# Performance work log

Hardware: AMD Instinct MI355X
Metric: run time of the kernel (lower is better)

## Reference

```python
import jax, jax.numpy as jnp
import numpy as np

B, H = 65536, 256  # batch, hidden_size (== input_size since combine = input + hidden)


def setup_inputs() -> dict:
    key = jax.random.key(0)
    ks = jax.random.split(key, 11)
    s = 1.0 / np.sqrt(H)  # nn.Linear default init scale
    return {
        "input": jax.random.normal(ks[0], (B, H), jnp.float32),
        "hidden": jax.random.normal(ks[1], (B, H), jnp.float32),
        "cell": jax.random.normal(ks[2], (B, H), jnp.float32),
        "Wf": jax.random.uniform(ks[3], (H, H), jnp.float32, -s, s),
        "bf": jax.random.uniform(ks[4], (H,), jnp.float32, -s, s),
        "Wc": jax.random.uniform(ks[5], (H, H), jnp.float32, -s, s),
        "bc": jax.random.uniform(ks[6], (H,), jnp.float32, -s, s),
        "Wi": jax.random.uniform(ks[7], (H, H), jnp.float32, -s, s),
        "bi": jax.random.uniform(ks[8], (H,), jnp.float32, -s, s),
        "Wo": jax.random.uniform(ks[9], (H, H), jnp.float32, -s, s),
        "bo": jax.random.uniform(ks[10], (H,), jnp.float32, -s, s),
    }


def reference(input, hidden, cell, Wf, bf, Wc, bc, Wi, bi, Wo, bo):
    combine = input + hidden                                   # [B, H]
    ft = jax.nn.sigmoid(combine @ Wf.T + bf)                   # forget gate
    ct_ = jnp.tanh(combine @ Wc.T + bc)                        # candidate
    it = jax.nn.sigmoid(jax.nn.sigmoid(combine @ Wi.T + bi))   # note: double sigmoid, as in source
    cell_state = cell * ft + ct_ * it                          # [B, H]
    out = jax.nn.sigmoid(combine @ Wo.T + bo)                  # output gate
    hidden_state = out * jnp.tanh(cell_state)
    return (out, hidden_state, cell_state)
```

## Files before the change

### kernel.cpp

```cpp
#include <hip/hip_runtime.h>
#include <hip/hip_bf16.h>


typedef __attribute__((ext_vector_type(8))) short short8;
typedef __attribute__((ext_vector_type(4))) float f32x4;

static constexpr int Bsz  = 65536;
static constexpr int Hdim = 256;

__device__ __forceinline__ short f2bf(float f) {
    unsigned u = __float_as_uint(f);
    return (short)((u + 0x7FFFu + ((u >> 16) & 1u)) >> 16);
}
__device__ __forceinline__ float fast_rcp(float x) {
    float r;
    asm("v_rcp_f32 %0, %1" : "=v"(r) : "v"(x));
    return r;
}
__device__ __forceinline__ float sigm(float x) {
    return fast_rcp(1.0f + __expf(-x));
}
__device__ __forceinline__ float tanh_fast(float x) {
    return 2.0f * fast_rcp(1.0f + __expf(-2.0f * x)) - 1.0f;
}

__global__ void __launch_bounds__(256)
prep_w_kernel(const float* __restrict__ Wf, const float* __restrict__ Wc,
              const float* __restrict__ Wi, const float* __restrict__ Wo,
              short* __restrict__ Bp)
{
    int o    = blockIdx.x * 256 + threadIdx.x;
    int e    = o & 7;
    int lane = (o >> 3) & 63;
    int jf   = (o >> 9) & 15;
    int ks   = (o >> 13) & 7;
    int g    = (o >> 16) & 3;
    int k = ks * 32 + (lane >> 4) * 8 + e;
    int j = jf * 16 + (lane & 15);
    const float* W = (g == 0) ? Wf : (g == 1) ? Wc : (g == 2) ? Wi : Wo;
    Bp[o] = f2bf(W[j * 256 + k]);
}

__global__ void __launch_bounds__(256, 4)
lstm_main(const float* __restrict__ inp, const float* __restrict__ hid,
          const float* __restrict__ cell, const short* __restrict__ Bp,
          const float* __restrict__ bfv, const float* __restrict__ bcv,
          const float* __restrict__ biv, const float* __restrict__ bov,
          float* __restrict__ out)
{
    __shared__ short As[32 * 256];

    const int tid  = threadIdx.x;
    const int lane = tid & 63;
    const int wave = tid >> 6;
    const int lm   = lane & 15;
    const int lk   = lane >> 4;

    const int bid     = blockIdx.x;
    const int jq      = (bid >> 3) & 3;
    const int rowtile = (bid >> 5) * 8 + (bid & 7);
    const int rowblk  = rowtile * 32;

    const int j         = jq * 64 + wave * 16 + lm;
    const int jf_global = jq * 4 + wave;

    float4 Li[4][2], Lh[4][2];
#pragma unroll
    for (int c = 0; c < 4; ++c) {
        int cc  = tid + c * 256;
        int row = cc >> 5;
        int k0  = (cc & 31) * 8;
        const float4* ip = reinterpret_cast<const float4*>(inp + (size_t)(rowblk + row) * Hdim + k0);
        const float4* hp = reinterpret_cast<const float4*>(hid + (size_t)(rowblk + row) * Hdim + k0);
        Li[c][0] = ip[0]; Li[c][1] = ip[1];
        Lh[c][0] = hp[0]; Lh[c][1] = hp[1];
    }
    float cv[2][4];
#pragma unroll
    for (int mf = 0; mf < 2; ++mf)
#pragma unroll
        for (int r = 0; r < 4; ++r)
            cv[mf][r] = cell[(size_t)(rowblk + mf * 16 + lk * 4 + r) * Hdim + j];
    const float bF = bfv[j], bC = bcv[j], bI = biv[j], bO = bov[j];

#pragma unroll
    for (int c = 0; c < 4; ++c) {
        int cc  = tid + c * 256;
        int row = cc >> 5;
        int k0  = (cc & 31) * 8;
        short8 v;
        v[0] = f2bf(Li[c][0].x + Lh[c][0].x);
        v[1] = f2bf(Li[c][0].y + Lh[c][0].y);
        v[2] = f2bf(Li[c][0].z + Lh[c][0].z);
        v[3] = f2bf(Li[c][0].w + Lh[c][0].w);
        v[4] = f2bf(Li[c][1].x + Lh[c][1].x);
        v[5] = f2bf(Li[c][1].y + Lh[c][1].y);
        v[6] = f2bf(Li[c][1].z + Lh[c][1].z);
        v[7] = f2bf(Li[c][1].w + Lh[c][1].w);
        int byte = (row * 512 + k0 * 2) ^ ((row & 7) << 4);
        *reinterpret_cast<short8*>(reinterpret_cast<char*>(As) + byte) = v;
    }

    __syncthreads();

    f32x4 acc[4][2];
    acc[0][0] = (f32x4){bF, bF, bF, bF};
    acc[1][0] = (f32x4){bC, bC, bC, bC};
    acc[2][0] = (f32x4){bI, bI, bI, bI};
    acc[3][0] = (f32x4){bO, bO, bO, bO};
#pragma unroll
    for (int g = 0; g < 4; ++g) acc[g][1] = acc[g][0];

    const char* A = reinterpret_cast<const char*>(As);
    auto wload = [&](int g, int ks) -> short8 {
        int chunk = (g * 8 + ks) * 16 + jf_global;
        return *reinterpret_cast<const short8*>(Bp + ((size_t)chunk * 64 + lane) * 8);
    };
    auto aload = [&](int mf, int ks) -> short8 {
        int row  = mf * 16 + lm;
        int byte = (row * 512 + (ks * 32 + lk * 8) * 2) ^ ((row & 7) << 4);
        return *reinterpret_cast<const short8*>(A + byte);
    };

    short8 bA0 = wload(0, 0), bA1 = wload(1, 0), bA2 = wload(2, 0), bA3 = wload(3, 0);

#pragma unroll
    for (int ks2 = 0; ks2 < 8; ks2 += 2) {
        short8 cf0[2] = { aload(0, ks2), aload(1, ks2) };
        short8 bB0 = wload(0, ks2 + 1), bB1 = wload(1, ks2 + 1),
               bB2 = wload(2, ks2 + 1), bB3 = wload(3, ks2 + 1);
        acc[0][0] = __builtin_amdgcn_mfma_f32_16x16x32_bf16(cf0[0], bA0, acc[0][0], 0, 0, 0);
        acc[0][1] = __builtin_amdgcn_mfma_f32_16x16x32_bf16(cf0[1], bA0, acc[0][1], 0, 0, 0);
        acc[1][0] = __builtin_amdgcn_mfma_f32_16x16x32_bf16(cf0[0], bA1, acc[1][0], 0, 0, 0);
        acc[1][1] = __builtin_amdgcn_mfma_f32_16x16x32_bf16(cf0[1], bA1, acc[1][1], 0, 0, 0);
        acc[2][0] = __builtin_amdgcn_mfma_f32_16x16x32_bf16(cf0[0], bA2, acc[2][0], 0, 0, 0);
        acc[2][1] = __builtin_amdgcn_mfma_f32_16x16x32_bf16(cf0[1], bA2, acc[2][1], 0, 0, 0);
        acc[3][0] = __builtin_amdgcn_mfma_f32_16x16x32_bf16(cf0[0], bA3, acc[3][0], 0, 0, 0);
        acc[3][1] = __builtin_amdgcn_mfma_f32_16x16x32_bf16(cf0[1], bA3, acc[3][1], 0, 0, 0);

        short8 cf1[2] = { aload(0, ks2 + 1), aload(1, ks2 + 1) };
        if (ks2 + 2 < 8) {
            bA0 = wload(0, ks2 + 2); bA1 = wload(1, ks2 + 2);
            bA2 = wload(2, ks2 + 2); bA3 = wload(3, ks2 + 2);
        }
        acc[0][0] = __builtin_amdgcn_mfma_f32_16x16x32_bf16(cf1[0], bB0, acc[0][0], 0, 0, 0);
        acc[0][1] = __builtin_amdgcn_mfma_f32_16x16x32_bf16(cf1[1], bB0, acc[0][1], 0, 0, 0);
        acc[1][0] = __builtin_amdgcn_mfma_f32_16x16x32_bf16(cf1[0], bB1, acc[1][0], 0, 0, 0);
        acc[1][1] = __builtin_amdgcn_mfma_f32_16x16x32_bf16(cf1[1], bB1, acc[1][1], 0, 0, 0);
        acc[2][0] = __builtin_amdgcn_mfma_f32_16x16x32_bf16(cf1[0], bB2, acc[2][0], 0, 0, 0);
        acc[2][1] = __builtin_amdgcn_mfma_f32_16x16x32_bf16(cf1[1], bB2, acc[2][1], 0, 0, 0);
        acc[3][0] = __builtin_amdgcn_mfma_f32_16x16x32_bf16(cf1[0], bB3, acc[3][0], 0, 0, 0);
        acc[3][1] = __builtin_amdgcn_mfma_f32_16x16x32_bf16(cf1[1], bB3, acc[3][1], 0, 0, 0);
    }

    float* out0 = out;
    float* out1 = out + (size_t)Bsz * Hdim;
    float* out2 = out + (size_t)2 * Bsz * Hdim;

#pragma unroll
    for (int mf = 0; mf < 2; ++mf) {
#pragma unroll
        for (int r = 0; r < 4; ++r) {
            int row = rowblk + mf * 16 + lk * 4 + r;
            size_t off = (size_t)row * Hdim + j;
            float F = sigm(acc[0][mf][r]);
            float C = tanh_fast(acc[1][mf][r]);
            float I = sigm(sigm(acc[2][mf][r]));
            float O = sigm(acc[3][mf][r]);
            float cs = cv[mf][r] * F + C * I;
            float hs = O * tanh_fast(cs);
            out0[off] = O;
            out1[off] = hs;
            out2[off] = cs;
        }
    }
}

extern "C" void kernel_launch(void* const* d_in, const int* in_sizes, int n_in,
                              void* d_out, int out_size, void* d_ws, size_t ws_size,
                              hipStream_t stream)
{
    const float* inp  = (const float*)d_in[0];
    const float* hid  = (const float*)d_in[1];
    const float* cell = (const float*)d_in[2];
    const float* Wf   = (const float*)d_in[3];
    const float* bf_  = (const float*)d_in[4];
    const float* Wc   = (const float*)d_in[5];
    const float* bc_  = (const float*)d_in[6];
    const float* Wi   = (const float*)d_in[7];
    const float* bi_  = (const float*)d_in[8];
    const float* Wo   = (const float*)d_in[9];
    const float* bo_  = (const float*)d_in[10];

    short* Bp = (short*)d_ws;

    prep_w_kernel<<<1024, 256, 0, stream>>>(Wf, Wc, Wi, Wo, Bp);
    lstm_main<<<(Bsz / 32) * 4, 256, 0, stream>>>(inp, hid, cell, Bp,
                                                  bf_, bc_, bi_, bo_, (float*)d_out);
}
```

Baseline: 143.2 us.

## Double row tile to 64 rows per block to reuse weight fragments

Each block now processes 64 batch rows instead of 32, loading the combined input in two rounds into a larger LDS tile and computing four M-fragments per weight load. This halves the weight fragment reads per output row and halves the block count. The software double-buffered weight prefetch is removed in favour of a simple per-ks loop. The cost is more accumulator registers and LDS, which may reduce occupancy, and the input loads are split into two rounds instead of being fully issued before the conversion.

```diff
diff --git a/kernel.cpp b/kernel.cpp
--- a/kernel.cpp
+++ b/kernel.cpp
@@ -48,7 +48,7 @@
           const float* __restrict__ biv, const float* __restrict__ bov,
           float* __restrict__ out)
 {
-    __shared__ short As[32 * 256];
+    __shared__ short As[64 * 256];
 
     const int tid  = threadIdx.x;
     const int lane = tid & 63;
@@ -59,98 +59,84 @@
     const int bid     = blockIdx.x;
     const int jq      = (bid >> 3) & 3;
     const int rowtile = (bid >> 5) * 8 + (bid & 7);
-    const int rowblk  = rowtile * 32;
+    const int rowblk  = rowtile * 64;
 
     const int j         = jq * 64 + wave * 16 + lm;
     const int jf_global = jq * 4 + wave;
 
-    float4 Li[4][2], Lh[4][2];
 #pragma unroll
-    for (int c = 0; c < 4; ++c) {
-        int cc  = tid + c * 256;
-        int row = cc >> 5;
-        int k0  = (cc & 31) * 8;
-        const float4* ip = reinterpret_cast<const float4*>(inp + (size_t)(rowblk + row) * Hdim + k0);
-        const float4* hp = reinterpret_cast<const float4*>(hid + (size_t)(rowblk + row) * Hdim + k0);
-        Li[c][0] = ip[0]; Li[c][1] = ip[1];
-        Lh[c][0] = hp[0]; Lh[c][1] = hp[1];
+    for (int round = 0; round < 2; ++round) {
+        float4 Li[4][2], Lh[4][2];
+#pragma unroll
+        for (int c = 0; c < 4; ++c) {
+            int cc  = tid + (round * 4 + c) * 256;
+            int row = cc >> 5;
+            int k0  = (cc & 31) * 8;
+            const float4* ip = reinterpret_cast<const float4*>(inp + (size_t)(rowblk + row) * Hdim + k0);
+            const float4* hp = reinterpret_cast<const float4*>(hid + (size_t)(rowblk + row) * Hdim + k0);
+            Li[c][0] = ip[0]; Li[c][1] = ip[1];
+            Lh[c][0] = hp[0]; Lh[c][1] = hp[1];
+        }
+#pragma unroll
+        for (int c = 0; c < 4; ++c) {
+            int cc  = tid + (round * 4 + c) * 256;
+            int row = cc >> 5;
+            int k0  = (cc & 31) * 8;
+            short8 v;
+            v[0] = f2bf(Li[c][0].x + Lh[c][0].x);
+            v[1] = f2bf(Li[c][0].y + Lh[c][0].y);
+            v[2] = f2bf(Li[c][0].z + Lh[c][0].z);
+            v[3] = f2bf(Li[c][0].w + Lh[c][0].w);
+            v[4] = f2bf(Li[c][1].x + Lh[c][1].x);
+            v[5] = f2bf(Li[c][1].y + Lh[c][1].y);
+            v[6] = f2bf(Li[c][1].z + Lh[c][1].z);
+            v[7] = f2bf(Li[c][1].w + Lh[c][1].w);
+            int byte = (row * 512 + k0 * 2) ^ ((row & 7) << 4);
+            *reinterpret_cast<short8*>(reinterpret_cast<char*>(As) + byte) = v;
+        }
     }
-    float cv[2][4];
+
+    float cv[4][4];
 #pragma unroll
-    for (int mf = 0; mf < 2; ++mf)
+    for (int mf = 0; mf < 4; ++mf)
 #pragma unroll
         for (int r = 0; r < 4; ++r)
             cv[mf][r] = cell[(size_t)(rowblk + mf * 16 + lk * 4 + r) * Hdim + j];
     const float bF = bfv[j], bC = bcv[j], bI = biv[j], bO = bov[j];
 
-#pragma unroll
-    for (int c = 0; c < 4; ++c) {
-        int cc  = tid + c * 256;
-        int row = cc >> 5;
-        int k0  = (cc & 31) * 8;
-        short8 v;
-        v[0] = f2bf(Li[c][0].x + Lh[c][0].x);
-        v[1] = f2bf(Li[c][0].y + Lh[c][0].y);
-        v[2] = f2bf(Li[c][0].z + Lh[c][0].z);
-        v[3] = f2bf(Li[c][0].w + Lh[c][0].w);
-        v[4] = f2bf(Li[c][1].x + Lh[c][1].x);
-        v[5] = f2bf(Li[c][1].y + Lh[c][1].y);
-        v[6] = f2bf(Li[c][1].z + Lh[c][1].z);
-        v[7] = f2bf(Li[c][1].w + Lh[c][1].w);
-        int byte = (row * 512 + k0 * 2) ^ ((row & 7) << 4);
-        *reinterpret_cast<short8*>(reinterpret_cast<char*>(As) + byte) = v;
-    }
-
     __syncthreads();
 
-    f32x4 acc[4][2];
+    f32x4 acc[4][4];
     acc[0][0] = (f32x4){bF, bF, bF, bF};
     acc[1][0] = (f32x4){bC, bC, bC, bC};
     acc[2][0] = (f32x4){bI, bI, bI, bI};
     acc[3][0] = (f32x4){bO, bO, bO, bO};
 #pragma unroll
-    for (int g = 0; g < 4; ++g) acc[g][1] = acc[g][0];
+    for (int g = 0; g < 4; ++g)
+#pragma unroll
+        for (int mf = 1; mf < 4; ++mf)
+            acc[g][mf] = acc[g][0];
 
     const char* A = reinterpret_cast<const char*>(As);
-    auto wload = [&](int g, int ks) -> short8 {
-        int chunk = (g * 8 + ks) * 16 + jf_global;
-        return *reinterpret_cast<const short8*>(Bp + ((size_t)chunk * 64 + lane) * 8);
-    };
-    auto aload = [&](int mf, int ks) -> short8 {
-        int row  = mf * 16 + lm;
-        int byte = (row * 512 + (ks * 32 + lk * 8) * 2) ^ ((row & 7) << 4);
-        return *reinterpret_cast<const short8*>(A + byte);
-    };
-
-    short8 bA0 = wload(0, 0), bA1 = wload(1, 0), bA2 = wload(2, 0), bA3 = wload(3, 0);
-
 #pragma unroll
-    for (int ks2 = 0; ks2 < 8; ks2 += 2) {
-        short8 cf0[2] = { aload(0, ks2), aload(1, ks2) };
-        short8 bB0 = wload(0, ks2 + 1), bB1 = wload(1, ks2 + 1),
-               bB2 = wload(2, ks2 + 1), bB3 = wload(3, ks2 + 1);
-        acc[0][0] = __builtin_amdgcn_mfma_f32_16x16x32_bf16(cf0[0], bA0, acc[0][0], 0, 0, 0);
-        acc[0][1] = __builtin_amdgcn_mfma_f32_16x16x32_bf16(cf0[1], bA0, acc[0][1], 0, 0, 0);
-        acc[1][0] = __builtin_amdgcn_mfma_f32_16x16x32_bf16(cf0[0], bA1, acc[1][0], 0, 0, 0);
-        acc[1][1] = __builtin_amdgcn_mfma_f32_16x16x32_bf16(cf0[1], bA1, acc[1][1], 0, 0, 0);
-        acc[2][0] = __builtin_amdgcn_mfma_f32_16x16x32_bf16(cf0[0], bA2, acc[2][0], 0, 0, 0);
-        acc[2][1] = __builtin_amdgcn_mfma_f32_16x16x32_bf16(cf0[1], bA2, acc[2][1], 0, 0, 0);
-        acc[3][0] = __builtin_amdgcn_mfma_f32_16x16x32_bf16(cf0[0], bA3, acc[3][0], 0, 0, 0);
-        acc[3][1] = __builtin_amdgcn_mfma_f32_16x16x32_bf16(cf0[1], bA3, acc[3][1], 0, 0, 0);
-
-        short8 cf1[2] = { aload(0, ks2 + 1), aload(1, ks2 + 1) };
-        if (ks2 + 2 < 8) {
-            bA0 = wload(0, ks2 + 2); bA1 = wload(1, ks2 + 2);
-            bA2 = wload(2, ks2 + 2); bA3 = wload(3, ks2 + 2);
+    for (int ks = 0; ks < 8; ++ks) {
+        short8 cf[4];
+#pragma unroll
+        for (int mf = 0; mf < 4; ++mf) {
+            int row  = mf * 16 + lm;
+            int byte = (row * 512 + (ks * 32 + lk * 8) * 2) ^ ((row & 7) << 4);
+            cf[mf] = *reinterpret_cast<const short8*>(A + byte);
         }
-        acc[0][0] = __builtin_amdgcn_mfma_f32_16x16x32_bf16(cf1[0], bB0, acc[0][0], 0, 0, 0);
-        acc[0][1] = __builtin_amdgcn_mfma_f32_16x16x32_bf16(cf1[1], bB0, acc[0][1], 0, 0, 0);
-        acc[1][0] = __builtin_amdgcn_mfma_f32_16x16x32_bf16(cf1[0], bB1, acc[1][0], 0, 0, 0);
-        acc[1][1] = __builtin_amdgcn_mfma_f32_16x16x32_bf16(cf1[1], bB1, acc[1][1], 0, 0, 0);
-        acc[2][0] = __builtin_amdgcn_mfma_f32_16x16x32_bf16(cf1[0], bB2, acc[2][0], 0, 0, 0);
-        acc[2][1] = __builtin_amdgcn_mfma_f32_16x16x32_bf16(cf1[1], bB2, acc[2][1], 0, 0, 0);
-        acc[3][0] = __builtin_amdgcn_mfma_f32_16x16x32_bf16(cf1[0], bB3, acc[3][0], 0, 0, 0);
-        acc[3][1] = __builtin_amdgcn_mfma_f32_16x16x32_bf16(cf1[1], bB3, acc[3][1], 0, 0, 0);
+#pragma unroll
+        for (int g = 0; g < 4; ++g) {
+            int chunk = (g * 8 + ks) * 16 + jf_global;
+            short8 b = *reinterpret_cast<const short8*>(
+                           Bp + ((size_t)chunk * 64 + lane) * 8);
+            acc[g][0] = __builtin_amdgcn_mfma_f32_16x16x32_bf16(cf[0], b, acc[g][0], 0, 0, 0);
+            acc[g][1] = __builtin_amdgcn_mfma_f32_16x16x32_bf16(cf[1], b, acc[g][1], 0, 0, 0);
+            acc[g][2] = __builtin_amdgcn_mfma_f32_16x16x32_bf16(cf[2], b, acc[g][2], 0, 0, 0);
+            acc[g][3] = __builtin_amdgcn_mfma_f32_16x16x32_bf16(cf[3], b, acc[g][3], 0, 0, 0);
+        }
     }
 
     float* out0 = out;
@@ -158,7 +144,7 @@
     float* out2 = out + (size_t)2 * Bsz * Hdim;
 
 #pragma unroll
-    for (int mf = 0; mf < 2; ++mf) {
+    for (int mf = 0; mf < 4; ++mf) {
 #pragma unroll
         for (int r = 0; r < 4; ++r) {
             int row = rowblk + mf * 16 + lk * 4 + r;
@@ -195,6 +181,6 @@
     short* Bp = (short*)d_ws;
 
     prep_w_kernel<<<1024, 256, 0, stream>>>(Wf, Wc, Wi, Wo, Bp);
-    lstm_main<<<(Bsz / 32) * 4, 256, 0, stream>>>(inp, hid, cell, Bp,
+    lstm_main<<<(Bsz / 64) * 4, 256, 0, stream>>>(inp, hid, cell, Bp,
                                                   bf_, bc_, bi_, bo_, (float*)d_out);
 }
```

Result: slower. 182.5 us (+27.5%).
